# Kernel tuning notes

Hardware: AMD Instinct MI355X
Metric: run time of the kernel (lower is better)

## Reference

```python
import jax, jax.numpy as jnp
import numpy as np
import math

LN_EPS = 1e-5

def setup_inputs() -> dict:
    key = jax.random.key(0)
    ks = jax.random.split(key, 8)
    B, S, D = 2, 2048, 2048
    sc = 1.0 / math.sqrt(D)
    return {
        "x": jax.random.normal(ks[0], (B, S, D), dtype=jnp.float32),
        "Wq": jax.random.normal(ks[1], (D, D), dtype=jnp.float32) * sc,
        "bq": jnp.zeros((D,), jnp.float32),
        "Wk": jax.random.normal(ks[2], (D, D), dtype=jnp.float32) * sc,
        "bk": jnp.zeros((D,), jnp.float32),
        "Wv": jax.random.normal(ks[3], (D, D), dtype=jnp.float32) * sc,
        "bv": jnp.zeros((D,), jnp.float32),
        "Wo": jax.random.normal(ks[4], (D, D), dtype=jnp.float32) * sc,
        "bo": jnp.zeros((D,), jnp.float32),
        "gamma": jnp.ones((D,), jnp.float32),
        "beta": jnp.zeros((D,), jnp.float32),
        "num_heads": 16,
    }

def reference(x, Wq, bq, Wk, bk, Wv, bv, Wo, bo, gamma, beta, num_heads):
    B, S, D = x.shape
    H = num_heads
    Dh = D // H
    # projections (torch Linear: y = x W^T + b; here W stored as [in,out])
    q = (x @ Wq + bq).reshape(B, S, H, Dh).transpose(0, 2, 1, 3)  # [B,H,S,Dh]
    k = (x @ Wk + bk).reshape(B, S, H, Dh).transpose(0, 2, 1, 3)
    v = (x @ Wv + bv).reshape(B, S, H, Dh).transpose(0, 2, 1, 3)
    scores = jnp.einsum("bhqd,bhkd->bhqk", q, k) / jnp.sqrt(jnp.asarray(Dh, x.dtype))
    causal = jnp.tril(jnp.ones((S, S), bool))  # [S,S]
    scores = jnp.where(causal[None, None], scores, -jnp.inf)
    # original subtracts row-max then softmax == stable softmax
    attn = jax.nn.softmax(scores, axis=-1)
    ctx = jnp.einsum("bhqk,bhkd->bhqd", attn, v)
    ctx = ctx.transpose(0, 2, 1, 3).reshape(B, S, D)
    attn_out = ctx @ Wo + bo
    y = attn_out + x
    mu = jnp.mean(y, axis=-1, keepdims=True)
    var = jnp.mean((y - mu) ** 2, axis=-1, keepdims=True)
    ln = gamma * (y - mu) * jax.lax.rsqrt(var + LN_EPS) + beta
    return (ln, attn_out, k, v)
```

## Files before the change

### kernel.cpp

```cpp
#include <hip/hip_runtime.h>
#include <hip/hip_bf16.h>
#include <math.h>
#include <stdint.h>

typedef __bf16 bf16;
typedef __bf16 bf16x4 __attribute__((ext_vector_type(4)));
typedef __bf16 bf16x8 __attribute__((ext_vector_type(8)));
typedef float f32x4 __attribute__((ext_vector_type(4)));

#define D_MODEL 2048
#define SEQ     2048
#define NHEADS  16
#define DH      128

__device__ __forceinline__ void async_copy16(const bf16* g, bf16* l) {
    typedef const unsigned int __attribute__((address_space(1))) gu32;
    typedef unsigned int __attribute__((address_space(3))) lu32;
    __builtin_amdgcn_global_load_lds((gu32*)g, (lu32*)(unsigned int)(unsigned long long)(l),
                                     16, 0, 0);
}

__global__ __launch_bounds__(256)
void convert_x_kernel(const float* __restrict__ x, bf16* __restrict__ xb)
{
    int i = blockIdx.x * 256 + threadIdx.x;
    float4 v = ((const float4*)x)[i];
    bf16x4 o;
    o[0] = (bf16)v.x; o[1] = (bf16)v.y; o[2] = (bf16)v.z; o[3] = (bf16)v.w;
    ((bf16x4*)xb)[i] = o;
}

__global__ __launch_bounds__(256)
void transpose_w_kernel(const float* __restrict__ Wq, const float* __restrict__ Wk,
                        const float* __restrict__ Wv, const float* __restrict__ Wo,
                        bf16* __restrict__ WTbase)
{
    const int z = blockIdx.z;
    const float* __restrict__ W = (z == 0) ? Wq : (z == 1) ? Wk : (z == 2) ? Wv : Wo;
    bf16* __restrict__ Wt = WTbase + (size_t)z * (D_MODEL * D_MODEL);
    const int n0 = blockIdx.x * 64, k0 = blockIdx.y * 64;
    const int tid = threadIdx.x;
    __shared__ bf16 Tl[64][68];

#pragma unroll
    for (int i = 0; i < 4; ++i) {
        int idx = tid + i * 256;
        int kr = idx >> 4, nc = (idx & 15) * 4;
        float4 w = *(const float4*)&W[(size_t)(k0 + kr) * D_MODEL + n0 + nc];
        Tl[nc + 0][kr] = (bf16)w.x;
        Tl[nc + 1][kr] = (bf16)w.y;
        Tl[nc + 2][kr] = (bf16)w.z;
        Tl[nc + 3][kr] = (bf16)w.w;
    }
    __syncthreads();
#pragma unroll
    for (int i = 0; i < 4; ++i) {
        int idx = tid + i * 256;
        int nr = idx >> 4, kc = (idx & 15) * 4;
        *(bf16x4*)&Wt[(size_t)(n0 + nr) * D_MODEL + k0 + kc] = *(const bf16x4*)&Tl[nr][kc];
    }
}

__global__ __launch_bounds__(256)
void transpose_v_kernel(const float* __restrict__ V, bf16* __restrict__ Vt)
{
    const int s0 = blockIdx.x * 64, d0 = blockIdx.y * 64, bh = blockIdx.z;
    const float* __restrict__ Vb = V + (size_t)bh * SEQ * DH;
    bf16* __restrict__ Vtb = Vt + (size_t)bh * DH * SEQ;
    const int tid = threadIdx.x;
    __shared__ bf16 Tl[64][68];

#pragma unroll
    for (int i = 0; i < 4; ++i) {
        int idx = tid + i * 256;
        int sr = idx >> 4, dc = (idx & 15) * 4;
        float4 v = *(const float4*)&Vb[(size_t)(s0 + sr) * DH + d0 + dc];
        Tl[dc + 0][sr] = (bf16)v.x;
        Tl[dc + 1][sr] = (bf16)v.y;
        Tl[dc + 2][sr] = (bf16)v.z;
        Tl[dc + 3][sr] = (bf16)v.w;
    }
    __syncthreads();
#pragma unroll
    for (int i = 0; i < 4; ++i) {
        int idx = tid + i * 256;
        int dr = idx >> 4, sc = (idx & 15) * 4;
        *(bf16x4*)&Vtb[(size_t)(d0 + dr) * SEQ + s0 + sc] = *(const bf16x4*)&Tl[dr][sc];
    }
}

__device__ __forceinline__ void gemm256_core(const bf16* __restrict__ A,
                                             const bf16* __restrict__ Bt,
                                             int bm, int bn,
                                             bf16* lds,
                                             f32x4 acc[8][4])
{
    const int tid = threadIdx.x;
    const int wave = tid >> 6, lane = tid & 63, quad = lane >> 4, l16 = lane & 15;
    const int wr = wave >> 2, wc = wave & 3;
    const int rowA = bm * 256, rowB = bn * 256;

    auto stageA = [&](int p, int kt, int h) {
#pragma unroll
        for (int j = 0; j < 2; ++j) {
            const int f = h * 16 + j * 8 + wave;
            const int mt = f >> 1, kk = f & 1;
            const bf16* g = &A[(size_t)(rowA + mt * 16 + l16) * D_MODEL + kt * 64 + kk * 32 + quad * 8];
            async_copy16(g, lds + p * 32768 + f * 512 + lane * 8);
        }
    };
    auto stageB = [&](int p, int kt, int h) {
#pragma unroll
        for (int j = 0; j < 2; ++j) {
            const int f = h * 16 + j * 8 + wave;
            const int nt = f >> 1, kk = f & 1;
            const bf16* g = &Bt[(size_t)(rowB + nt * 16 + l16) * D_MODEL + kt * 64 + kk * 32 + quad * 8];
            async_copy16(g, lds + p * 32768 + 16384 + f * 512 + lane * 8);
        }
    };

    stageA(0, 0, 0); stageA(0, 0, 1);
    stageB(0, 0, 0); stageB(0, 0, 1);
    stageB(1, 1, 0); stageB(1, 1, 1);
    asm volatile("s_waitcnt vmcnt(4)" ::: "memory");
    __builtin_amdgcn_s_barrier();

    for (int t = 0; t < 32; ++t) {
        const int p = t & 1;
        const bf16* Ab = lds + p * 32768;
        const bf16* Bb = Ab + 16384;
        const int tn1 = (t + 1 < 31) ? t + 1 : 31;
        const int tn2 = (t + 2 < 31) ? t + 2 : 31;
        bf16x8 bfr[4][2];
#pragma unroll
        for (int q = 0; q < 4; ++q) {
            bf16x8 af[2][2];
#pragma unroll
            for (int mi = 0; mi < 2; ++mi)
#pragma unroll
                for (int kk = 0; kk < 2; ++kk) {
                    const int mt = wr * 8 + 2 * q + mi;
                    af[mi][kk] = *(const bf16x8*)(Ab + (mt * 2 + kk) * 512 + lane * 8);
                }
            if (q == 0) {
#pragma unroll
                for (int n = 0; n < 4; ++n)
#pragma unroll
                    for (int kk = 0; kk < 2; ++kk) {
                        const int nt = wc * 4 + n;
                        bfr[n][kk] = *(const bf16x8*)(Bb + (nt * 2 + kk) * 512 + lane * 8);
                    }
                stageA(p ^ 1, tn1, 0);
            } else if (q == 1) {
                stageA(p ^ 1, tn1, 1);
            } else if (q == 2) {
                stageB(p, tn2, 0);
            } else {
                stageB(p, tn2, 1);
            }

            __builtin_amdgcn_s_barrier();
            asm volatile("s_waitcnt lgkmcnt(0)" ::: "memory");
            __builtin_amdgcn_sched_barrier(0);
            __builtin_amdgcn_s_setprio(1);
#pragma unroll
            for (int mi = 0; mi < 2; ++mi)
#pragma unroll
                for (int n = 0; n < 4; ++n)
#pragma unroll
                    for (int kk = 0; kk < 2; ++kk)
                        acc[2 * q + mi][n] = __builtin_amdgcn_mfma_f32_16x16x32_bf16(
                            af[mi][kk], bfr[n][kk], acc[2 * q + mi][n], 0, 0, 0);
            __builtin_amdgcn_s_setprio(0);
            if (q == 3) asm volatile("s_waitcnt vmcnt(4)" ::: "memory");
            __builtin_amdgcn_s_barrier();
        }
    }
    asm volatile("s_waitcnt vmcnt(0)" ::: "memory");
}

__global__ __launch_bounds__(512, 2)
void gemm_qkv_kernel(const bf16* __restrict__ A, const bf16* __restrict__ WT,
                     const float* __restrict__ bq, const float* __restrict__ bk,
                     const float* __restrict__ bv,
                     bf16* __restrict__ qout, float* __restrict__ kout,
                     bf16* __restrict__ kb16, float* __restrict__ vout)
{
    __shared__ bf16 lds[65536];
    const int id = blockIdx.x;
    const int swz = (id & 7) * 48 + (id >> 3);
    const int bm = swz / 24, bn = swz % 24;

    f32x4 acc[8][4] = {};
    gemm256_core(A, WT, bm, bn, lds, acc);

    const int tid = threadIdx.x;
    const int wave = tid >> 6, lane = tid & 63, quad = lane >> 4, l16 = lane & 15;
    const int wr = wave >> 2, wc = wave & 3;
    const int z = bn >> 3;
    const float* __restrict__ bias = (z == 0) ? bq : (z == 1) ? bk : bv;

#pragma unroll
    for (int mi = 0; mi < 8; ++mi) {
#pragma unroll
        for (int n = 0; n < 4; ++n) {
#pragma unroll
            for (int r = 0; r < 4; ++r) {
                int m  = bm * 256 + wr * 128 + mi * 16 + quad * 4 + r;
                int nl = (bn & 7) * 256 + wc * 64 + n * 16 + l16;
                float val = acc[mi][n][r] + bias[nl];
                int b = m >> 11, s = m & (SEQ - 1);
                int h = nl >> 7, dh = nl & (DH - 1);
                size_t off = ((size_t)(b * NHEADS + h) * SEQ + s) * DH + dh;
                if (z == 0) {
                    qout[off] = (bf16)val;
                } else if (z == 1) {
                    kout[off] = val;
                    kb16[off] = (bf16)val;
                } else {
                    vout[off] = val;
                }
            }
        }
    }
}

__global__ __launch_bounds__(512, 2)
void gemm_out_kernel(const bf16* __restrict__ A, const bf16* __restrict__ Bt,
                     const float* __restrict__ bias, float* __restrict__ out)
{
    __shared__ bf16 lds[65536];
    const int id = blockIdx.x;
    const int swz = (id & 7) * 16 + (id >> 3);
    const int bm = swz >> 3, bn = swz & 7;

    f32x4 acc[8][4] = {};
    gemm256_core(A, Bt, bm, bn, lds, acc);

    const int tid = threadIdx.x;
    const int wave = tid >> 6, lane = tid & 63, quad = lane >> 4, l16 = lane & 15;
    const int wr = wave >> 2, wc = wave & 3;

#pragma unroll
    for (int mi = 0; mi < 8; ++mi) {
#pragma unroll
        for (int n = 0; n < 4; ++n) {
#pragma unroll
            for (int r = 0; r < 4; ++r) {
                int m = bm * 256 + wr * 128 + mi * 16 + quad * 4 + r;
                int nn = bn * 256 + wc * 64 + n * 16 + l16;
                out[(size_t)m * D_MODEL + nn] = acc[mi][n][r] + bias[nn];
            }
        }
    }
}

__global__ __launch_bounds__(256, 4)
void attn_kernel(const bf16* __restrict__ Q, const bf16* __restrict__ K,
                 const bf16* __restrict__ Vt, bf16* __restrict__ ctx)
{
    const int id = blockIdx.x;
    const int p  = id & 511;
    const int bh = p >> 4;
    const int j  = p & 15;
    const int qb = (id >> 9) ? j : (31 - j);

    const int tid = threadIdx.x;
    const int wave = tid >> 6, lane = tid & 63, quad = lane >> 4, l16 = lane & 15;

    __shared__ bf16 Ks[64 * 128];
    __shared__ bf16 VsT[128 * 64];
    __shared__ bf16 Ps[4 * 16 * 64];
    char* const ksb = (char*)Ks;
    char* const vsb = (char*)VsT;
    char* const psb = (char*)Ps + wave * 2048;

    const bf16* qsrc = Q + ((size_t)bh * SEQ + (size_t)qb * 64 + wave * 16 + l16) * DH;
    bf16x8 qf[4];
#pragma unroll
    for (int dd = 0; dd < 4; ++dd)
        qf[dd] = *(const bf16x8*)&qsrc[dd * 32 + quad * 8];

    f32x4 o[8] = {};
    float m_i[4], l_i[4];
#pragma unroll
    for (int r = 0; r < 4; ++r) { m_i[r] = -INFINITY; l_i[r] = 0.f; }

    const float scale = 0.08838834764831845f;
    const bf16* ksrc0 = K + (size_t)bh * SEQ * DH;
    const bf16* vsrc0 = Vt + (size_t)bh * DH * SEQ;

    for (int kb = 0; kb <= qb; ++kb) {
        __syncthreads();

        {
            const char* kg = (const char*)(ksrc0 + (size_t)(kb * 64) * DH);
#pragma unroll
            for (int i = 0; i < 4; ++i) {
                int seg = i * 4 + wave;
                int row = seg * 4 + (lane >> 4);
                int colb = (lane & 15) * 16;
                const char* src = kg + row * 256 + (colb ^ ((row & 7) << 4));
                async_copy16((const bf16*)src, (bf16*)(ksb + seg * 1024));
            }
            const char* vg = (const char*)(vsrc0 + kb * 64);
#pragma unroll
            for (int i = 0; i < 4; ++i) {
                int seg = i * 4 + wave;
                int d = seg * 8 + (lane >> 3);
                int colb = (lane & 7) * 16;
                const char* src = vg + (size_t)d * (SEQ * 2) + (colb ^ ((d & 7) << 4));
                async_copy16((const bf16*)src, (bf16*)(vsb + seg * 1024));
            }
        }
        __syncthreads();

        float pvals[4][4];
#pragma unroll
        for (int t = 0; t < 4; ++t) {
            f32x4 s = {};
            const int row = t * 16 + l16;
            const int swz = (row & 7) << 4;
#pragma unroll
            for (int dd = 0; dd < 4; ++dd) {
                bf16x8 b = *(const bf16x8*)(ksb + row * 256 + ((dd * 64 + quad * 16) ^ swz));
                s = __builtin_amdgcn_mfma_f32_16x16x32_bf16(qf[dd], b, s, 0, 0, 0);
            }
#pragma unroll
            for (int r = 0; r < 4; ++r) pvals[t][r] = s[r];
        }

        const bool diag = (kb == qb);
#pragma unroll
        for (int r = 0; r < 4; ++r) {
            int qrow = qb * 64 + wave * 16 + quad * 4 + r;
            float mx = -INFINITY;
#pragma unroll
            for (int t = 0; t < 4; ++t) {
                float s = pvals[t][r] * scale;
                int kcol = kb * 64 + t * 16 + l16;
                if (diag && kcol > qrow) s = -INFINITY;
                pvals[t][r] = s;
                mx = fmaxf(mx, s);
            }
#pragma unroll
            for (int off = 1; off < 16; off <<= 1)
                mx = fmaxf(mx, __shfl_xor(mx, off, 64));
            float mnew = fmaxf(m_i[r], mx);
            float alpha = __expf(m_i[r] - mnew);
            m_i[r] = mnew;
            float rs = 0.f;
#pragma unroll
            for (int t = 0; t < 4; ++t) {
                float pexp = __expf(pvals[t][r] - mnew);
                pvals[t][r] = pexp;
                rs += pexp;
            }
#pragma unroll
            for (int off = 1; off < 16; off <<= 1)
                rs += __shfl_xor(rs, off, 64);
            l_i[r] = l_i[r] * alpha + rs;
#pragma unroll
            for (int dt = 0; dt < 8; ++dt) o[dt][r] *= alpha;
        }

#pragma unroll
        for (int t = 0; t < 4; ++t)
#pragma unroll
            for (int r = 0; r < 4; ++r) {
                int row = quad * 4 + r;
                *(bf16*)(psb + row * 128 + (((t * 16 + l16) * 2) ^ ((row & 7) << 4))) =
                    (bf16)pvals[t][r];
            }

        bf16x8 pa[2];
#pragma unroll
        for (int kk2 = 0; kk2 < 2; ++kk2)
            pa[kk2] = *(const bf16x8*)(psb + l16 * 128 +
                                       ((kk2 * 64 + quad * 16) ^ ((l16 & 7) << 4)));
#pragma unroll
        for (int dt = 0; dt < 8; ++dt) {
            const int row = dt * 16 + l16;
            const int swz = (row & 7) << 4;
#pragma unroll
            for (int kk2 = 0; kk2 < 2; ++kk2) {
                bf16x8 b = *(const bf16x8*)(vsb + row * 128 + ((kk2 * 64 + quad * 16) ^ swz));
                o[dt] = __builtin_amdgcn_mfma_f32_16x16x32_bf16(pa[kk2], b, o[dt], 0, 0, 0);
            }
        }
    }

    const int b = bh >> 4, h = bh & (NHEADS - 1);
    float inv_l[4];
#pragma unroll
    for (int r = 0; r < 4; ++r) inv_l[r] = 1.0f / l_i[r];
#pragma unroll
    for (int dt = 0; dt < 8; ++dt) {
#pragma unroll
        for (int r = 0; r < 4; ++r) {
            int s = qb * 64 + wave * 16 + quad * 4 + r;
            int d = dt * 16 + l16;
            ctx[((size_t)(b * SEQ + s)) * D_MODEL + h * DH + d] = (bf16)(o[dt][r] * inv_l[r]);
        }
    }
}

__global__ __launch_bounds__(256)
void ln_kernel(const float* __restrict__ attn, const float* __restrict__ x,
               const float* __restrict__ gamma, const float* __restrict__ beta,
               float* __restrict__ ln)
{
    const int row = blockIdx.x;
    const int tid = threadIdx.x;
    const int wave = tid >> 6, lane = tid & 63;
    const float* a  = attn + (size_t)row * D_MODEL;
    const float* xr = x    + (size_t)row * D_MODEL;

    float4 y4[2];
    float sum = 0.f, sumsq = 0.f;
#pragma unroll
    for (int i = 0; i < 2; ++i) {
        int c = (tid + i * 256) * 4;
        float4 av = *(const float4*)&a[c];
        float4 xv = *(const float4*)&xr[c];
        float4 y;
        y.x = av.x + xv.x; y.y = av.y + xv.y; y.z = av.z + xv.z; y.w = av.w + xv.w;
        y4[i] = y;
        sum   += y.x + y.y + y.z + y.w;
        sumsq += y.x * y.x + y.y * y.y + y.z * y.z + y.w * y.w;
    }
#pragma unroll
    for (int off = 1; off < 64; off <<= 1) {
        sum   += __shfl_xor(sum, off, 64);
        sumsq += __shfl_xor(sumsq, off, 64);
    }
    __shared__ float rsum[4], rsumsq[4];
    if (lane == 0) { rsum[wave] = sum; rsumsq[wave] = sumsq; }
    __syncthreads();
    float tot = 0.f, tot2 = 0.f;
#pragma unroll
    for (int i = 0; i < 4; ++i) { tot += rsum[i]; tot2 += rsumsq[i]; }
    const float mu  = tot * (1.0f / D_MODEL);
    const float var = tot2 * (1.0f / D_MODEL) - mu * mu;
    const float rstd = rsqrtf(var + 1e-5f);

#pragma unroll
    for (int i = 0; i < 2; ++i) {
        int c = (tid + i * 256) * 4;
        float4 gv = *(const float4*)&gamma[c];
        float4 bv = *(const float4*)&beta[c];
        float4 y = y4[i];
        float4 r;
        r.x = gv.x * (y.x - mu) * rstd + bv.x;
        r.y = gv.y * (y.y - mu) * rstd + bv.y;
        r.z = gv.z * (y.z - mu) * rstd + bv.z;
        r.w = gv.w * (y.w - mu) * rstd + bv.w;
        *(float4*)&ln[(size_t)row * D_MODEL + c] = r;
    }
}

extern "C" void kernel_launch(void* const* d_in, const int* in_sizes, int n_in,
                              void* d_out, int out_size, void* d_ws, size_t ws_size,
                              hipStream_t stream)
{
    const float* x     = (const float*)d_in[0];
    const float* Wq    = (const float*)d_in[1];
    const float* bq    = (const float*)d_in[2];
    const float* Wk    = (const float*)d_in[3];
    const float* bk    = (const float*)d_in[4];
    const float* Wv    = (const float*)d_in[5];
    const float* bv    = (const float*)d_in[6];
    const float* Wo    = (const float*)d_in[7];
    const float* bo    = (const float*)d_in[8];
    const float* gamma = (const float*)d_in[9];
    const float* beta  = (const float*)d_in[10];

    float* out      = (float*)d_out;
    float* ln       = out;
    float* attn_out = out + 8388608;
    float* kout     = out + 16777216;
    float* vout     = out + 25165824;

    bf16* wsb  = (bf16*)d_ws;
    bf16* xb   = wsb;
    bf16* WT   = wsb + 8388608;
    bf16* qws  = wsb + 25165824;
    bf16* kb16 = wsb + 33554432;
    bf16* vT   = wsb + 41943040;
    bf16* ctx  = wsb + 50331648;

    convert_x_kernel<<<8192, 256, 0, stream>>>(x, xb);
    transpose_w_kernel<<<dim3(32, 32, 4), 256, 0, stream>>>(Wq, Wk, Wv, Wo, WT);
    gemm_qkv_kernel<<<dim3(384), 512, 0, stream>>>(xb, WT, bq, bk, bv,
                                                    qws, kout, kb16, vout);
    transpose_v_kernel<<<dim3(32, 2, 32), 256, 0, stream>>>(vout, vT);
    attn_kernel<<<dim3(1024), 256, 0, stream>>>(qws, kb16, vT, ctx);
    gemm_out_kernel<<<dim3(128), 512, 0, stream>>>(ctx, WT + 3 * (size_t)(D_MODEL * D_MODEL),
                                                    bo, attn_out);
    ln_kernel<<<4096, 256, 0, stream>>>(attn_out, x, gamma, beta, ln);
}
```

Before: 582.0 us.

## Shrink GEMM tiles to 128x256 to double block count for better CU occupancy

```diff
diff --git a/kernel.cpp b/kernel.cpp
--- a/kernel.cpp
+++ b/kernel.cpp
@@ -89,92 +89,102 @@
     }
 }
 
-__device__ __forceinline__ void gemm256_core(const bf16* __restrict__ A,
-                                             const bf16* __restrict__ Bt,
-                                             int bm, int bn,
-                                             bf16* lds,
-                                             f32x4 acc[8][4])
+__device__ __forceinline__ void gemm128x256_core(const bf16* __restrict__ A,
+                                                 const bf16* __restrict__ Bt,
+                                                 int bm, int bn,
+                                                 bf16* lds,
+                                                 f32x4 acc[4][4])
 {
     const int tid = threadIdx.x;
     const int wave = tid >> 6, lane = tid & 63, quad = lane >> 4, l16 = lane & 15;
     const int wr = wave >> 2, wc = wave & 3;
-    const int rowA = bm * 256, rowB = bn * 256;
-
-    auto stageA = [&](int p, int kt, int h) {
-#pragma unroll
-        for (int j = 0; j < 2; ++j) {
-            const int f = h * 16 + j * 8 + wave;
-            const int mt = f >> 1, kk = f & 1;
-            const bf16* g = &A[(size_t)(rowA + mt * 16 + l16) * D_MODEL + kt * 64 + kk * 32 + quad * 8];
-            async_copy16(g, lds + p * 32768 + f * 512 + lane * 8);
-        }
+
+    const bf16* pA[2]; int dA[2];
+#pragma unroll
+    for (int j = 0; j < 2; ++j) {
+        const int f = j * 8 + wave;
+        pA[j] = A + (size_t)(bm * 128 + (f >> 1) * 16 + l16) * D_MODEL + (f & 1) * 32 + quad * 8;
+        dA[j] = f * 512 + lane * 8;
+    }
+    const bf16* pB[4]; int dB[4];
+#pragma unroll
+    for (int i = 0; i < 4; ++i) {
+        const int f = (i >> 1) * 16 + (i & 1) * 8 + wave;
+        pB[i] = Bt + (size_t)(bn * 256 + (f >> 1) * 16 + l16) * D_MODEL + (f & 1) * 32 + quad * 8;
+        dB[i] = f * 512 + lane * 8;
+    }
+
+    auto stA = [&](int p, int kt) {
+#pragma unroll
+        for (int j = 0; j < 2; ++j)
+            async_copy16(pA[j] + kt * 64, lds + p * 24576 + dA[j]);
     };
-    auto stageB = [&](int p, int kt, int h) {
-#pragma unroll
-        for (int j = 0; j < 2; ++j) {
-            const int f = h * 16 + j * 8 + wave;
-            const int nt = f >> 1, kk = f & 1;
-            const bf16* g = &Bt[(size_t)(rowB + nt * 16 + l16) * D_MODEL + kt * 64 + kk * 32 + quad * 8];
-            async_copy16(g, lds + p * 32768 + 16384 + f * 512 + lane * 8);
-        }
+    auto stB = [&](int p, int kt, int h) {
+#pragma unroll
+        for (int j = 0; j < 2; ++j)
+            async_copy16(pB[h * 2 + j] + kt * 64, lds + p * 24576 + 8192 + dB[h * 2 + j]);
     };
 
-    stageA(0, 0, 0); stageA(0, 0, 1);
-    stageB(0, 0, 0); stageB(0, 0, 1);
-    stageB(1, 1, 0); stageB(1, 1, 1);
+    stA(0, 0); stB(0, 0, 0); stB(0, 0, 1); stB(1, 1, 0); stB(1, 1, 1);
     asm volatile("s_waitcnt vmcnt(4)" ::: "memory");
     __builtin_amdgcn_s_barrier();
 
     for (int t = 0; t < 32; ++t) {
         const int p = t & 1;
-        const bf16* Ab = lds + p * 32768;
-        const bf16* Bb = Ab + 16384;
+        const bf16* Ab = lds + p * 24576;
+        const bf16* Bb = Ab + 8192;
         const int tn1 = (t + 1 < 31) ? t + 1 : 31;
         const int tn2 = (t + 2 < 31) ? t + 2 : 31;
-        bf16x8 bfr[4][2];
-#pragma unroll
-        for (int q = 0; q < 4; ++q) {
-            bf16x8 af[2][2];
-#pragma unroll
-            for (int mi = 0; mi < 2; ++mi)
-#pragma unroll
-                for (int kk = 0; kk < 2; ++kk) {
-                    const int mt = wr * 8 + 2 * q + mi;
-                    af[mi][kk] = *(const bf16x8*)(Ab + (mt * 2 + kk) * 512 + lane * 8);
-                }
-            if (q == 0) {
-#pragma unroll
-                for (int n = 0; n < 4; ++n)
-#pragma unroll
-                    for (int kk = 0; kk < 2; ++kk) {
-                        const int nt = wc * 4 + n;
-                        bfr[n][kk] = *(const bf16x8*)(Bb + (nt * 2 + kk) * 512 + lane * 8);
-                    }
-                stageA(p ^ 1, tn1, 0);
-            } else if (q == 1) {
-                stageA(p ^ 1, tn1, 1);
-            } else if (q == 2) {
-                stageB(p, tn2, 0);
-            } else {
-                stageB(p, tn2, 1);
-            }
-
-            __builtin_amdgcn_s_barrier();
-            asm volatile("s_waitcnt lgkmcnt(0)" ::: "memory");
-            __builtin_amdgcn_sched_barrier(0);
-            __builtin_amdgcn_s_setprio(1);
-#pragma unroll
-            for (int mi = 0; mi < 2; ++mi)
-#pragma unroll
-                for (int n = 0; n < 4; ++n)
-#pragma unroll
-                    for (int kk = 0; kk < 2; ++kk)
-                        acc[2 * q + mi][n] = __builtin_amdgcn_mfma_f32_16x16x32_bf16(
-                            af[mi][kk], bfr[n][kk], acc[2 * q + mi][n], 0, 0, 0);
-            __builtin_amdgcn_s_setprio(0);
-            if (q == 3) asm volatile("s_waitcnt vmcnt(4)" ::: "memory");
-            __builtin_amdgcn_s_barrier();
-        }
+
+        bf16x8 bfr[4][2], af[2][2];
+
+#pragma unroll
+        for (int mi = 0; mi < 2; ++mi)
+#pragma unroll
+            for (int kk = 0; kk < 2; ++kk)
+                af[mi][kk] = *(const bf16x8*)(Ab + ((wr * 4 + mi) * 2 + kk) * 512 + lane * 8);
+#pragma unroll
+        for (int n = 0; n < 4; ++n)
+#pragma unroll
+            for (int kk = 0; kk < 2; ++kk)
+                bfr[n][kk] = *(const bf16x8*)(Bb + ((wc * 4 + n) * 2 + kk) * 512 + lane * 8);
+        stA(p ^ 1, tn1);
+        __builtin_amdgcn_s_barrier();
+        asm volatile("s_waitcnt lgkmcnt(0)" ::: "memory");
+        __builtin_amdgcn_sched_barrier(0);
+        __builtin_amdgcn_s_setprio(1);
+#pragma unroll
+        for (int mi = 0; mi < 2; ++mi)
+#pragma unroll
+            for (int n = 0; n < 4; ++n)
+#pragma unroll
+                for (int kk = 0; kk < 2; ++kk)
+                    acc[mi][n] = __builtin_amdgcn_mfma_f32_16x16x32_bf16(
+                        af[mi][kk], bfr[n][kk], acc[mi][n], 0, 0, 0);
+        __builtin_amdgcn_s_setprio(0);
+        __builtin_amdgcn_s_barrier();
+
+#pragma unroll
+        for (int mi = 0; mi < 2; ++mi)
+#pragma unroll
+            for (int kk = 0; kk < 2; ++kk)
+                af[mi][kk] = *(const bf16x8*)(Ab + ((wr * 4 + 2 + mi) * 2 + kk) * 512 + lane * 8);
+        stB(p, tn2, 0); stB(p, tn2, 1);
+        __builtin_amdgcn_s_barrier();
+        asm volatile("s_waitcnt lgkmcnt(0)" ::: "memory");
+        __builtin_amdgcn_sched_barrier(0);
+        __builtin_amdgcn_s_setprio(1);
+#pragma unroll
+        for (int mi = 0; mi < 2; ++mi)
+#pragma unroll
+            for (int n = 0; n < 4; ++n)
+#pragma unroll
+                for (int kk = 0; kk < 2; ++kk)
+                    acc[2 + mi][n] = __builtin_amdgcn_mfma_f32_16x16x32_bf16(
+                        af[mi][kk], bfr[n][kk], acc[2 + mi][n], 0, 0, 0);
+        __builtin_amdgcn_s_setprio(0);
+        asm volatile("s_waitcnt vmcnt(4)" ::: "memory");
+        __builtin_amdgcn_s_barrier();
     }
     asm volatile("s_waitcnt vmcnt(0)" ::: "memory");
 }
@@ -186,13 +196,13 @@
                      bf16* __restrict__ qout, float* __restrict__ kout,
                      bf16* __restrict__ kb16, float* __restrict__ vout)
 {
-    __shared__ bf16 lds[65536];
+    __shared__ bf16 lds[49152];
     const int id = blockIdx.x;
-    const int swz = (id & 7) * 48 + (id >> 3);
-    const int bm = swz / 24, bn = swz % 24;
-
-    f32x4 acc[8][4] = {};
-    gemm256_core(A, WT, bm, bn, lds, acc);
+    const int swz = (id & 7) * 96 + (id >> 3);
+    const int bm = swz & 31, bn = swz >> 5;
+
+    f32x4 acc[4][4] = {};
+    gemm128x256_core(A, WT, bm, bn, lds, acc);
 
     const int tid = threadIdx.x;
     const int wave = tid >> 6, lane = tid & 63, quad = lane >> 4, l16 = lane & 15;
@@ -201,14 +211,14 @@
     const float* __restrict__ bias = (z == 0) ? bq : (z == 1) ? bk : bv;
 
 #pragma unroll
-    for (int mi = 0; mi < 8; ++mi) {
+    for (int a = 0; a < 4; ++a) {
 #pragma unroll
         for (int n = 0; n < 4; ++n) {
 #pragma unroll
             for (int r = 0; r < 4; ++r) {
-                int m  = bm * 256 + wr * 128 + mi * 16 + quad * 4 + r;
+                int m  = bm * 128 + wr * 64 + a * 16 + quad * 4 + r;
                 int nl = (bn & 7) * 256 + wc * 64 + n * 16 + l16;
-                float val = acc[mi][n][r] + bias[nl];
+                float val = acc[a][n][r] + bias[nl];
                 int b = m >> 11, s = m & (SEQ - 1);
                 int h = nl >> 7, dh = nl & (DH - 1);
                 size_t off = ((size_t)(b * NHEADS + h) * SEQ + s) * DH + dh;
@@ -229,27 +239,27 @@
 void gemm_out_kernel(const bf16* __restrict__ A, const bf16* __restrict__ Bt,
                      const float* __restrict__ bias, float* __restrict__ out)
 {
-    __shared__ bf16 lds[65536];
+    __shared__ bf16 lds[49152];
     const int id = blockIdx.x;
-    const int swz = (id & 7) * 16 + (id >> 3);
-    const int bm = swz >> 3, bn = swz & 7;
-
-    f32x4 acc[8][4] = {};
-    gemm256_core(A, Bt, bm, bn, lds, acc);
+    const int swz = (id & 7) * 32 + (id >> 3);
+    const int bm = swz & 31, bn = swz >> 5;
+
+    f32x4 acc[4][4] = {};
+    gemm128x256_core(A, Bt, bm, bn, lds, acc);
 
     const int tid = threadIdx.x;
     const int wave = tid >> 6, lane = tid & 63, quad = lane >> 4, l16 = lane & 15;
     const int wr = wave >> 2, wc = wave & 3;
 
 #pragma unroll
-    for (int mi = 0; mi < 8; ++mi) {
+    for (int a = 0; a < 4; ++a) {
 #pragma unroll
         for (int n = 0; n < 4; ++n) {
 #pragma unroll
             for (int r = 0; r < 4; ++r) {
-                int m = bm * 256 + wr * 128 + mi * 16 + quad * 4 + r;
+                int m  = bm * 128 + wr * 64 + a * 16 + quad * 4 + r;
                 int nn = bn * 256 + wc * 64 + n * 16 + l16;
-                out[(size_t)m * D_MODEL + nn] = acc[mi][n][r] + bias[nn];
+                out[(size_t)m * D_MODEL + nn] = acc[a][n][r] + bias[nn];
             }
         }
     }
@@ -491,11 +501,11 @@
 
     convert_x_kernel<<<8192, 256, 0, stream>>>(x, xb);
     transpose_w_kernel<<<dim3(32, 32, 4), 256, 0, stream>>>(Wq, Wk, Wv, Wo, WT);
-    gemm_qkv_kernel<<<dim3(384), 512, 0, stream>>>(xb, WT, bq, bk, bv,
+    gemm_qkv_kernel<<<dim3(768), 512, 0, stream>>>(xb, WT, bq, bk, bv,
                                                     qws, kout, kb16, vout);
     transpose_v_kernel<<<dim3(32, 2, 32), 256, 0, stream>>>(vout, vT);
     attn_kernel<<<dim3(1024), 256, 0, stream>>>(qws, kb16, vT, ctx);
-    gemm_out_kernel<<<dim3(128), 512, 0, stream>>>(ctx, WT + 3 * (size_t)(D_MODEL * D_MODEL),
+    gemm_out_kernel<<<dim3(256), 512, 0, stream>>>(ctx, WT + 3 * (size_t)(D_MODEL * D_MODEL),
                                                     bo, attn_out);
     ln_kernel<<<4096, 256, 0, stream>>>(attn_out, x, gamma, beta, ln);
 }
```

Result: slower. 595.9 us (+2.4%).

## Use 256x192 tiles in QKV GEMM to fill a single wave of blocks

Applied to the files above, without the earlier changes.

```diff
diff --git a/kernel.cpp b/kernel.cpp
--- a/kernel.cpp
+++ b/kernel.cpp
@@ -87,6 +87,105 @@
         int dr = idx >> 4, sc = (idx & 15) * 4;
         *(bf16x4*)&Vtb[(size_t)(d0 + dr) * SEQ + s0 + sc] = *(const bf16x4*)&Tl[dr][sc];
     }
+}
+
+__device__ __forceinline__ void gemm256x192_core(const bf16* __restrict__ A,
+                                                 const bf16* __restrict__ Bt,
+                                                 int bm, int bn,
+                                                 bf16* lds,
+                                                 f32x4 acc[8][3])
+{
+    const int tid = threadIdx.x;
+    const int wave = tid >> 6, lane = tid & 63, quad = lane >> 4, l16 = lane & 15;
+    const int wr = wave >> 2, wc = wave & 3;
+
+    const bf16* pA[4]; int dA[4];
+#pragma unroll
+    for (int h = 0; h < 2; ++h)
+#pragma unroll
+        for (int j = 0; j < 2; ++j) {
+            const int f = h * 16 + j * 8 + wave;
+            pA[h * 2 + j] = A + (size_t)(bm * 256 + (f >> 1) * 16 + l16) * D_MODEL
+                              + (f & 1) * 32 + quad * 8;
+            dA[h * 2 + j] = f * 512 + lane * 8;
+        }
+    const bf16* pB[3]; int dB[3];
+#pragma unroll
+    for (int part = 0; part < 3; ++part) {
+        const int f = part * 8 + wave;
+        pB[part] = Bt + (size_t)(bn * 192 + (f >> 1) * 16 + l16) * D_MODEL
+                      + (f & 1) * 32 + quad * 8;
+        dB[part] = 16384 + f * 512 + lane * 8;
+    }
+
+    auto stA = [&](int p, int kt, int h) {
+#pragma unroll
+        for (int j = 0; j < 2; ++j)
+            async_copy16(pA[h * 2 + j] + kt * 64, lds + p * 28672 + dA[h * 2 + j]);
+    };
+    auto stB = [&](int p, int kt, int part) {
+        async_copy16(pB[part] + kt * 64, lds + p * 28672 + dB[part]);
+    };
+
+    stA(0, 0, 0); stA(0, 0, 1);
+    stB(0, 0, 0); stB(0, 0, 1); stB(0, 0, 2);
+    stB(1, 1, 0); stB(1, 1, 1); stB(1, 1, 2);
+    asm volatile("s_waitcnt vmcnt(3)" ::: "memory");
+    __builtin_amdgcn_s_barrier();
+
+    for (int t = 0; t < 32; ++t) {
+        const int p = t & 1;
+        const bf16* Ab = lds + p * 28672;
+        const bf16* Bb = Ab + 16384;
+        const int tn1 = (t + 1 < 31) ? t + 1 : 31;
+        const int tn2 = (t + 2 < 31) ? t + 2 : 31;
+        bf16x8 bfr[3][2];
+#pragma unroll
+        for (int q = 0; q < 4; ++q) {
+            bf16x8 af[2][2];
+#pragma unroll
+            for (int mi = 0; mi < 2; ++mi)
+#pragma unroll
+                for (int kk = 0; kk < 2; ++kk) {
+                    const int mt = wr * 8 + 2 * q + mi;
+                    af[mi][kk] = *(const bf16x8*)(Ab + (mt * 2 + kk) * 512 + lane * 8);
+                }
+            if (q == 0) {
+#pragma unroll
+                for (int n = 0; n < 3; ++n)
+#pragma unroll
+                    for (int kk = 0; kk < 2; ++kk) {
+                        const int nt = wc * 3 + n;
+                        bfr[n][kk] = *(const bf16x8*)(Bb + (nt * 2 + kk) * 512 + lane * 8);
+                    }
+                stA(p ^ 1, tn1, 0);
+            } else if (q == 1) {
+                stA(p ^ 1, tn1, 1);
+                stB(p, tn2, 0);
+            } else if (q == 2) {
+                stB(p, tn2, 1);
+            } else {
+                stB(p, tn2, 2);
+            }
+
+            __builtin_amdgcn_s_barrier();
+            asm volatile("s_waitcnt lgkmcnt(0)" ::: "memory");
+            __builtin_amdgcn_sched_barrier(0);
+            __builtin_amdgcn_s_setprio(1);
+#pragma unroll
+            for (int mi = 0; mi < 2; ++mi)
+#pragma unroll
+                for (int n = 0; n < 3; ++n)
+#pragma unroll
+                    for (int kk = 0; kk < 2; ++kk)
+                        acc[2 * q + mi][n] = __builtin_amdgcn_mfma_f32_16x16x32_bf16(
+                            af[mi][kk], bfr[n][kk], acc[2 * q + mi][n], 0, 0, 0);
+            __builtin_amdgcn_s_setprio(0);
+            if (q == 3) asm volatile("s_waitcnt vmcnt(3)" ::: "memory");
+            __builtin_amdgcn_s_barrier();
+        }
+    }
+    asm volatile("s_waitcnt vmcnt(0)" ::: "memory");
 }
 
 __device__ __forceinline__ void gemm256_core(const bf16* __restrict__ A,
@@ -186,31 +285,32 @@
                      bf16* __restrict__ qout, float* __restrict__ kout,
                      bf16* __restrict__ kb16, float* __restrict__ vout)
 {
-    __shared__ bf16 lds[65536];
+    __shared__ bf16 lds[57344];
     const int id = blockIdx.x;
-    const int swz = (id & 7) * 48 + (id >> 3);
-    const int bm = swz / 24, bn = swz % 24;
-
-    f32x4 acc[8][4] = {};
-    gemm256_core(A, WT, bm, bn, lds, acc);
+    const int swz = (id & 7) * 64 + (id >> 3);
+    const int bm = swz >> 5, bn = swz & 31;
+
+    f32x4 acc[8][3] = {};
+    gemm256x192_core(A, WT, bm, bn, lds, acc);
 
     const int tid = threadIdx.x;
     const int wave = tid >> 6, lane = tid & 63, quad = lane >> 4, l16 = lane & 15;
     const int wr = wave >> 2, wc = wave & 3;
-    const int z = bn >> 3;
-    const float* __restrict__ bias = (z == 0) ? bq : (z == 1) ? bk : bv;
-
-#pragma unroll
-    for (int mi = 0; mi < 8; ++mi) {
-#pragma unroll
-        for (int n = 0; n < 4; ++n) {
+
+#pragma unroll
+    for (int a = 0; a < 8; ++a) {
+#pragma unroll
+        for (int n = 0; n < 3; ++n) {
+            const int col0 = bn * 192 + wc * 48 + n * 16;
+            const int z = col0 >> 11;
+            const float* __restrict__ bias = (z == 0) ? bq : (z == 1) ? bk : bv;
+            const int nl = (col0 & 2047) + l16;
+            const int h = nl >> 7, dh = nl & (DH - 1);
 #pragma unroll
             for (int r = 0; r < 4; ++r) {
-                int m  = bm * 256 + wr * 128 + mi * 16 + quad * 4 + r;
-                int nl = (bn & 7) * 256 + wc * 64 + n * 16 + l16;
-                float val = acc[mi][n][r] + bias[nl];
+                int m = bm * 256 + wr * 128 + a * 16 + quad * 4 + r;
+                float val = acc[a][n][r] + bias[nl];
                 int b = m >> 11, s = m & (SEQ - 1);
-                int h = nl >> 7, dh = nl & (DH - 1);
                 size_t off = ((size_t)(b * NHEADS + h) * SEQ + s) * DH + dh;
                 if (z == 0) {
                     qout[off] = (bf16)val;
@@ -491,7 +591,7 @@
 
     convert_x_kernel<<<8192, 256, 0, stream>>>(x, xb);
     transpose_w_kernel<<<dim3(32, 32, 4), 256, 0, stream>>>(Wq, Wk, Wv, Wo, WT);
-    gemm_qkv_kernel<<<dim3(384), 512, 0, stream>>>(xb, WT, bq, bk, bv,
+    gemm_qkv_kernel<<<dim3(512), 512, 0, stream>>>(xb, WT, bq, bk, bv,
                                                     qws, kout, kb16, vout);
     transpose_v_kernel<<<dim3(32, 2, 32), 256, 0, stream>>>(vout, vT);
     attn_kernel<<<dim3(1024), 256, 0, stream>>>(qws, kb16, vT, ctx);
```

New measurement: 566.1 us. 2.7% less time.
